# Optimization experiments

Measured on AMD Instinct MI355X. Metric: run time of the kernel, lower is better.

Reference implementation:

```python
import jax, jax.numpy as jnp
import numpy as np

N_NODES = 100000
N_EDGES = 600000
IN_FEATS = 128
HIDDEN = 128


def sage_conv(x, src, dst, w_l, b_l, w_r, num_nodes):
    """PyG SAGEConv with mean aggregation.
    out = mean_{j in N(i)} x_j @ w_l.T + b_l + x_i @ w_r.T
    src/dst: int arrays [E]; messages flow src -> dst.
    """
    msgs = x[src]                                             # [E, F] gather
    summed = jax.ops.segment_sum(msgs, dst, num_segments=num_nodes)  # [N, F]
    ones = jnp.ones((src.shape[0],), dtype=x.dtype)
    deg = jax.ops.segment_sum(ones, dst, num_segments=num_nodes)     # [N]
    agg = summed / jnp.maximum(deg, 1.0)[:, None]             # mean, safe for deg=0
    return agg @ w_l.T + b_l + x @ w_r.T


def setup_inputs() -> dict:
    key = jax.random.key(0)
    ks = jax.random.split(key, 10)

    def glorot(k, shape):
        fan_in = shape[-1]
        bound = 1.0 / np.sqrt(fan_in)
        return jax.random.uniform(k, shape, jnp.float32, -bound, bound)

    x = jax.random.normal(ks[0], (N_NODES, IN_FEATS), dtype=jnp.float32)
    xedge = jax.random.randint(ks[1], (2, N_EDGES), 0, N_NODES, dtype=jnp.int64)
    return {
        "x": x,
        "xedge": xedge,
        # SAGEConv 1 (in_feats -> hidden): lin_l (with bias) + lin_r (no bias)
        "w1_l": glorot(ks[2], (HIDDEN, IN_FEATS)),
        "b1_l": glorot(ks[3], (HIDDEN,)),
        "w1_r": glorot(ks[4], (HIDDEN, IN_FEATS)),
        # SAGEConv 2 (hidden -> hidden)
        "w2_l": glorot(ks[5], (HIDDEN, HIDDEN)),
        "b2_l": glorot(ks[6], (HIDDEN,)),
        "w2_r": glorot(ks[7], (HIDDEN, HIDDEN)),
        # Decoder: Linear(hidden -> hidden)
        "w_dec": glorot(ks[8], (HIDDEN, HIDDEN)),
        "b_dec": glorot(ks[9], (HIDDEN,)),
    }


def reference(x, xedge, w1_l, b1_l, w1_r, w2_l, b2_l, w2_r, w_dec, b_dec):
    src, dst = xedge[0], xedge[1]
    n = x.shape[0]
    h = sage_conv(x, src, dst, w1_l, b1_l, w1_r, n)   # conv1
    h = jax.nn.relu(h)
    # dropout omitted (deterministic eval semantics)
    h = sage_conv(h, src, dst, w2_l, b2_l, w2_r, n)   # conv2 -> encoder output
    dx = h @ w_dec.T + b_dec                          # decoder
    return (h, dx)
```

## Files before the change

### kernel.cpp

```cpp
#include <hip/hip_runtime.h>

typedef __attribute__((ext_vector_type(8))) short bf16x8;
typedef __attribute__((ext_vector_type(4))) float f32x4;
typedef unsigned int uint;
typedef unsigned short ushort;

#define NFEAT 128

__device__ __forceinline__ ushort f2b(float f) {
    uint u = __float_as_uint(f);
    u = (u + 0x7fffu + ((u >> 16) & 1u)) >> 16;
    return (ushort)u;
}

__global__ __launch_bounds__(256) void prep(
    const float* __restrict__ x, ushort* __restrict__ x_bf, long nx,
    const float* __restrict__ w1l, const float* __restrict__ w1r,
    const float* __restrict__ w2l, const float* __restrict__ w2r,
    const float* __restrict__ wd,
    ushort* __restrict__ wc1, ushort* __restrict__ wc2, ushort* __restrict__ wdec,
    const int* __restrict__ dst, int* __restrict__ deg, int E, int nCvt)
{
    const int b = blockIdx.x;
    if (b < nCvt) {
        long i = ((long)b * 256 + threadIdx.x) * 4;
        if (i < nx) {
            float4 v = *(const float4*)(x + i);
            ushort4 o;
            o.x = f2b(v.x); o.y = f2b(v.y); o.z = f2b(v.z); o.w = f2b(v.w);
            *(ushort4*)(x_bf + i) = o;
        }
    } else if (b < nCvt + 256) {
        const int bb = b - nCvt;
        const int i = (bb & 127) * 256 + threadIdx.x;
        const int row = i >> 8, col = i & 255;
        const float* wl = (bb < 128) ? w1l : w2l;
        const float* wr = (bb < 128) ? w1r : w2r;
        ushort* dstw = (bb < 128) ? wc1 : wc2;
        float v = (col < 128) ? wl[row * 128 + col] : wr[row * 128 + col - 128];
        dstw[i] = f2b(v);
    } else if (b < nCvt + 320) {
        const int i = (b - nCvt - 256) * 256 + threadIdx.x;
        wdec[i] = f2b(wd[i]);
    } else {
        const int e = (b - nCvt - 320) * 256 + threadIdx.x;
        if (e < E) atomicAdd(&deg[dst[e]], 1);
    }
}

__global__ __launch_bounds__(256) void scan_blocks(const int* __restrict__ in, int* __restrict__ out,
                                                   int* __restrict__ bsum, int n) {
    __shared__ int lds[256];
    const int t = threadIdx.x;
    const int base = blockIdx.x * 1024 + t * 4;
    int a[4];
#pragma unroll
    for (int q = 0; q < 4; ++q) a[q] = (base + q < n) ? in[base + q] : 0;
    const int tsum = a[0] + a[1] + a[2] + a[3];
    lds[t] = tsum;
    __syncthreads();
    for (int off = 1; off < 256; off <<= 1) {
        int v = (t >= off) ? lds[t - off] : 0;
        __syncthreads();
        lds[t] += v;
        __syncthreads();
    }
    const int excl = lds[t] - tsum;
    if (t == 255) bsum[blockIdx.x] = lds[255];
    int r = excl;
#pragma unroll
    for (int q = 0; q < 4; ++q) {
        if (base + q < n) out[base + q] = r;
        r += a[q];
    }
}

__global__ __launch_bounds__(256) void scan_add(int* __restrict__ row_off, int* __restrict__ pos,
                                                const int* __restrict__ bsum, int n, int E) {
    const int i = blockIdx.x * 256 + threadIdx.x;
    const int cb = blockIdx.x >> 2;
    const int lane = threadIdx.x & 63;
    int v = 0;
    if (lane < cb) v += bsum[lane];
    if (lane + 64 < cb) v += bsum[lane + 64];
#pragma unroll
    for (int off = 1; off < 64; off <<= 1) v += __shfl_xor(v, off);
    if (i < n) {
        const int r = row_off[i] + v;
        row_off[i] = r;
        pos[i] = r;
    }
    if (i == 0) row_off[n] = E;
}

__global__ void fill_csr(const int* __restrict__ src, const int* __restrict__ dst,
                         int* __restrict__ pos, int* __restrict__ perm, int E) {
    const int e = blockIdx.x * blockDim.x + threadIdx.x;
    if (e < E) {
        const int p = atomicAdd(&pos[dst[e]], 1);
        perm[p] = src[e];
    }
}

__global__ __launch_bounds__(256) void gather_mean_bf(const int* __restrict__ row_off,
                                                      const int* __restrict__ perm,
                                                      const ushort* __restrict__ feat,
                                                      ushort* __restrict__ out, int n) {
    const int node = (blockIdx.x * 256 + threadIdx.x) >> 4;
    if (node >= n) return;
    const int chunk = threadIdx.x & 15;
    const int lo = row_off[node], hi = row_off[node + 1];
    float acc[8] = {0.f, 0.f, 0.f, 0.f, 0.f, 0.f, 0.f, 0.f};
    int i = lo;
    for (; i + 3 < hi; i += 4) {
        const int s0 = perm[i], s1 = perm[i + 1], s2 = perm[i + 2], s3 = perm[i + 3];
        const uint4 v0 = *(const uint4*)(feat + (size_t)s0 * NFEAT + chunk * 8);
        const uint4 v1 = *(const uint4*)(feat + (size_t)s1 * NFEAT + chunk * 8);
        const uint4 v2 = *(const uint4*)(feat + (size_t)s2 * NFEAT + chunk * 8);
        const uint4 v3 = *(const uint4*)(feat + (size_t)s3 * NFEAT + chunk * 8);
        const uint p0[4] = {v0.x, v0.y, v0.z, v0.w};
        const uint p1[4] = {v1.x, v1.y, v1.z, v1.w};
        const uint p2[4] = {v2.x, v2.y, v2.z, v2.w};
        const uint p3[4] = {v3.x, v3.y, v3.z, v3.w};
#pragma unroll
        for (int q = 0; q < 4; ++q) {
            acc[2 * q]     += __uint_as_float(p0[q] << 16) + __uint_as_float(p1[q] << 16)
                            + __uint_as_float(p2[q] << 16) + __uint_as_float(p3[q] << 16);
            acc[2 * q + 1] += __uint_as_float(p0[q] & 0xffff0000u) + __uint_as_float(p1[q] & 0xffff0000u)
                            + __uint_as_float(p2[q] & 0xffff0000u) + __uint_as_float(p3[q] & 0xffff0000u);
        }
    }
    for (; i < hi; ++i) {
        const int s = perm[i];
        const uint4 v = *(const uint4*)(feat + (size_t)s * NFEAT + chunk * 8);
        const uint p[4] = {v.x, v.y, v.z, v.w};
#pragma unroll
        for (int q = 0; q < 4; ++q) {
            acc[2 * q]     += __uint_as_float(p[q] << 16);
            acc[2 * q + 1] += __uint_as_float(p[q] & 0xffff0000u);
        }
    }
    const float inv = 1.0f / fmaxf((float)(hi - lo), 1.0f);
    ushort o[8] __attribute__((aligned(16)));
#pragma unroll
    for (int q = 0; q < 8; ++q) o[q] = f2b(acc[q] * inv);
    *(uint4*)(out + (size_t)node * NFEAT + chunk * 8) = *(const uint4*)o;
}

template <bool RELU, bool DEC>
__global__ __launch_bounds__(256) void sage_mfma(
    const ushort* __restrict__ Amean, const ushort* __restrict__ Axin,
    const ushort* __restrict__ Wcat, const float* __restrict__ bias,
    const ushort* __restrict__ Wdec, const float* __restrict__ bdec,
    float* __restrict__ outf, ushort* __restrict__ outb,
    float* __restrict__ dxp, int n)
{
    __shared__ uint4 LhBuf[DEC ? 2048 : 1];
    char* Lh = (char*)LhBuf;
    const int t = threadIdx.x;
    const int m0 = blockIdx.x * 128;
    const int lane = t & 63;
    const int wid = t >> 6;
    const int lrow = lane & 15;
    const int lq = lane >> 4;

    int ar[2];
#pragma unroll
    for (int m = 0; m < 2; ++m) {
        int r = m0 + wid * 32 + m * 16 + lrow;
        ar[m] = (r < n) ? r : (n - 1);
    }

    f32x4 acc[2][8];
#pragma unroll
    for (int m = 0; m < 2; ++m)
#pragma unroll
        for (int nn = 0; nn < 8; ++nn) acc[m][nn] = (f32x4){0.f, 0.f, 0.f, 0.f};

#pragma unroll
    for (int kt = 0; kt < 4; ++kt) {
        const ushort* Abase = (kt < 2) ? Amean : Axin;
        const int co = (kt & 1) * 64;
#pragma unroll
        for (int ks = 0; ks < 2; ++ks) {
            const int kcol = co + ks * 32 + lq * 8;
            bf16x8 af[2], bfr[8];
#pragma unroll
            for (int m = 0; m < 2; ++m)
                af[m] = *(const bf16x8*)(Abase + (size_t)ar[m] * NFEAT + kcol);
#pragma unroll
            for (int nn = 0; nn < 8; ++nn)
                bfr[nn] = *(const bf16x8*)(Wcat + (size_t)(nn * 16 + lrow) * 256 + kt * 64 + ks * 32 + lq * 8);
#pragma unroll
            for (int m = 0; m < 2; ++m)
#pragma unroll
                for (int nn = 0; nn < 8; ++nn)
                    acc[m][nn] = __builtin_amdgcn_mfma_f32_16x16x32_bf16(bfr[nn], af[m], acc[m][nn], 0, 0, 0);
        }
    }

#pragma unroll
    for (int m = 0; m < 2; ++m) {
        const int row = wid * 32 + m * 16 + lrow;
        const int grow = m0 + row;
#pragma unroll
        for (int nn = 0; nn < 8; ++nn) {
            const int colb = nn * 16 + lq * 4;
            const float4 bv = *(const float4*)(bias + colb);
            float v0 = acc[m][nn][0] + bv.x;
            float v1 = acc[m][nn][1] + bv.y;
            float v2 = acc[m][nn][2] + bv.z;
            float v3 = acc[m][nn][3] + bv.w;
            if (RELU) {
                v0 = fmaxf(v0, 0.f); v1 = fmaxf(v1, 0.f);
                v2 = fmaxf(v2, 0.f); v3 = fmaxf(v3, 0.f);
            }
            ushort4 ob;
            ob.x = f2b(v0); ob.y = f2b(v1); ob.z = f2b(v2); ob.w = f2b(v3);
            if (grow < n) {
                if (outf) *(float4*)(outf + (size_t)grow * NFEAT + colb) = make_float4(v0, v1, v2, v3);
                if (outb) *(ushort4*)(outb + (size_t)grow * NFEAT + colb) = ob;
            }
            if (DEC)
                *(ushort4*)(Lh + row * 256 + ((colb * 2) ^ ((row & 7) << 4))) = ob;
        }
    }
    if (DEC) {
        f32x4 acc2[2][8];
#pragma unroll
        for (int m = 0; m < 2; ++m)
#pragma unroll
            for (int nn = 0; nn < 8; ++nn) acc2[m][nn] = (f32x4){0.f, 0.f, 0.f, 0.f};
#pragma unroll
        for (int ks = 0; ks < 4; ++ks) {
            bf16x8 af2[2], bf2[8];
#pragma unroll
            for (int m = 0; m < 2; ++m) {
                const int row = wid * 32 + m * 16 + lrow;
                af2[m] = *(const bf16x8*)(Lh + row * 256 + ((ks * 64 + lq * 16) ^ ((row & 7) << 4)));
            }
#pragma unroll
            for (int nn = 0; nn < 8; ++nn)
                bf2[nn] = *(const bf16x8*)(Wdec + (size_t)(nn * 16 + lrow) * NFEAT + ks * 32 + lq * 8);
#pragma unroll
            for (int m = 0; m < 2; ++m)
#pragma unroll
                for (int nn = 0; nn < 8; ++nn)
                    acc2[m][nn] = __builtin_amdgcn_mfma_f32_16x16x32_bf16(bf2[nn], af2[m], acc2[m][nn], 0, 0, 0);
        }
#pragma unroll
        for (int m = 0; m < 2; ++m) {
            const int grow = m0 + wid * 32 + m * 16 + lrow;
            if (grow < n) {
#pragma unroll
                for (int nn = 0; nn < 8; ++nn) {
                    const int colb = nn * 16 + lq * 4;
                    const float4 bv = *(const float4*)(bdec + colb);
                    *(float4*)(dxp + (size_t)grow * NFEAT + colb) =
                        make_float4(acc2[m][nn][0] + bv.x, acc2[m][nn][1] + bv.y,
                                    acc2[m][nn][2] + bv.z, acc2[m][nn][3] + bv.w);
                }
            }
        }
    }
}

extern "C" void kernel_launch(void* const* d_in, const int* in_sizes, int n_in,
                              void* d_out, int out_size, void* d_ws, size_t ws_size,
                              hipStream_t stream) {
    const float* x     = (const float*)d_in[0];
    const int*   xedge = (const int*)d_in[1];
    const float* w1_l  = (const float*)d_in[2];
    const float* b1_l  = (const float*)d_in[3];
    const float* w1_r  = (const float*)d_in[4];
    const float* w2_l  = (const float*)d_in[5];
    const float* b2_l  = (const float*)d_in[6];
    const float* w2_r  = (const float*)d_in[7];
    const float* w_dec = (const float*)d_in[8];
    const float* b_dec = (const float*)d_in[9];

    const int N = in_sizes[0] / NFEAT;
    const int E = in_sizes[1] / 2;
    const int* src = xedge;
    const int* dst = xedge + E;

    float* h_out = (float*)d_out;
    float* dxp   = h_out + (size_t)N * NFEAT;

    char* ws = (char*)d_ws;
    ushort* x_bf    = (ushort*)ws;
    ushort* h1_bf   = x_bf   + (size_t)N * NFEAT;
    ushort* mean_bf = h1_bf  + (size_t)N * NFEAT;
    ushort* wc1     = mean_bf + (size_t)N * NFEAT;
    ushort* wc2     = wc1 + 128 * 256;
    ushort* wdec    = wc2 + 128 * 256;
    int* deg        = (int*)(wdec + 128 * 128);
    int* row_off    = deg + N;
    int* pos        = row_off + (N + 1);
    int* bsum       = pos + N;
    int* perm       = bsum + 256;

    hipMemsetAsync(deg, 0, (size_t)N * sizeof(int), stream);
    const long nx = (long)N * NFEAT;
    const int nCvt = (int)((nx / 4 + 255) / 256);
    const int histB = (E + 255) / 256;
    prep<<<nCvt + 320 + histB, 256, 0, stream>>>(x, x_bf, nx, w1_l, w1_r, w2_l, w2_r, w_dec,
                                                 wc1, wc2, wdec, dst, deg, E, nCvt);

    const int nb = (N + 1023) / 1024;
    scan_blocks<<<nb, 256, 0, stream>>>(deg, row_off, bsum, N);
    scan_add<<<(N + 255) / 256, 256, 0, stream>>>(row_off, pos, bsum, N, E);
    fill_csr<<<histB, 256, 0, stream>>>(src, dst, pos, perm, E);

    const int gb = (N + 127) / 128;
    const int ggb = (N * 16 + 255) / 256;

    gather_mean_bf<<<ggb, 256, 0, stream>>>(row_off, perm, x_bf, mean_bf, N);
    sage_mfma<true, false><<<gb, 256, 0, stream>>>(mean_bf, x_bf, wc1, b1_l,
                                                   nullptr, nullptr, nullptr, h1_bf, nullptr, N);

    gather_mean_bf<<<ggb, 256, 0, stream>>>(row_off, perm, h1_bf, mean_bf, N);
    sage_mfma<false, true><<<gb, 256, 0, stream>>>(mean_bf, h1_bf, wc2, b2_l,
                                                   wdec, b_dec, h_out, nullptr, dxp, N);

    (void)n_in; (void)out_size; (void)ws_size;
}
```

Baseline: 245.0 us.

## Stage A and weight tiles into swizzled LDS via direct global-to-LDS loads

The MFMA GEMM kernel used to load A-row fragments and weight fragments straight from global memory into registers for each k-step. It now stages a 128x64 A tile and a 128x64 weight tile per k-tile into LDS with global_load_lds, using an XOR swizzle to avoid bank conflicts, then reads the MFMA fragments from LDS. The aim is coalesced, shared weight loads instead of each wave re-fetching the weights. In exchange it adds two barriers per k-tile with no double buffering, and it always allocates 32KB of LDS, which may lower occupancy.

Result: faster. 199.8 us (median of 3 runs) (-18.5%).

```diff
diff --git a/kernel.cpp b/kernel.cpp
--- a/kernel.cpp
+++ b/kernel.cpp
@@ -11,6 +11,11 @@
     uint u = __float_as_uint(f);
     u = (u + 0x7fffu + ((u >> 16) & 1u)) >> 16;
     return (ushort)u;
+}
+
+__device__ __forceinline__ void gload_lds16(const ushort* g, char* lds) {
+    __builtin_amdgcn_global_load_lds((const __attribute__((address_space(1))) void*)g,
+                                     (__attribute__((address_space(3))) void*)lds, 16, 0, 0);
 }
 
 __global__ __launch_bounds__(256) void prep(
@@ -155,8 +160,9 @@
     float* __restrict__ outf, ushort* __restrict__ outb,
     float* __restrict__ dxp, int n)
 {
-    __shared__ uint4 LhBuf[DEC ? 2048 : 1];
-    char* Lh = (char*)LhBuf;
+    __shared__ uint4 smem4[2048];
+    char* As = (char*)smem4;
+    char* Ws = As + 16384;
     const int t = threadIdx.x;
     const int m0 = blockIdx.x * 128;
     const int lane = t & 63;
@@ -164,41 +170,49 @@
     const int lrow = lane & 15;
     const int lq = lane >> 4;
 
-    int ar[2];
-#pragma unroll
-    for (int m = 0; m < 2; ++m) {
-        int r = m0 + wid * 32 + m * 16 + lrow;
-        ar[m] = (r < n) ? r : (n - 1);
-    }
-
     f32x4 acc[2][8];
 #pragma unroll
     for (int m = 0; m < 2; ++m)
 #pragma unroll
         for (int nn = 0; nn < 8; ++nn) acc[m][nn] = (f32x4){0.f, 0.f, 0.f, 0.f};
 
-#pragma unroll
     for (int kt = 0; kt < 4; ++kt) {
         const ushort* Abase = (kt < 2) ? Amean : Axin;
         const int co = (kt & 1) * 64;
 #pragma unroll
+        for (int i = 0; i < 4; ++i) {
+            const int row = i * 32 + wid * 8 + (lane >> 3);
+            const int c = (lane & 7) ^ (row & 7);
+            int gm = m0 + row;
+            if (gm >= n) gm = n - 1;
+            gload_lds16(Abase + (size_t)gm * NFEAT + co + c * 8,
+                        As + i * 4096 + wid * 1024);
+            gload_lds16(Wcat + (size_t)row * 256 + kt * 64 + c * 8,
+                        Ws + i * 4096 + wid * 1024);
+        }
+        __syncthreads();
+#pragma unroll
         for (int ks = 0; ks < 2; ++ks) {
-            const int kcol = co + ks * 32 + lq * 8;
             bf16x8 af[2], bfr[8];
 #pragma unroll
-            for (int m = 0; m < 2; ++m)
-                af[m] = *(const bf16x8*)(Abase + (size_t)ar[m] * NFEAT + kcol);
-#pragma unroll
-            for (int nn = 0; nn < 8; ++nn)
-                bfr[nn] = *(const bf16x8*)(Wcat + (size_t)(nn * 16 + lrow) * 256 + kt * 64 + ks * 32 + lq * 8);
+            for (int m = 0; m < 2; ++m) {
+                const int row = wid * 32 + m * 16 + lrow;
+                af[m] = *(const bf16x8*)(As + row * 128 + (((ks * 4 + lq) * 16) ^ ((row & 7) << 4)));
+            }
+#pragma unroll
+            for (int nn = 0; nn < 8; ++nn) {
+                const int row = nn * 16 + lrow;
+                bfr[nn] = *(const bf16x8*)(Ws + row * 128 + (((ks * 4 + lq) * 16) ^ ((row & 7) << 4)));
+            }
 #pragma unroll
             for (int m = 0; m < 2; ++m)
 #pragma unroll
                 for (int nn = 0; nn < 8; ++nn)
                     acc[m][nn] = __builtin_amdgcn_mfma_f32_16x16x32_bf16(bfr[nn], af[m], acc[m][nn], 0, 0, 0);
         }
-    }
-
+        __syncthreads();
+    }
+    char* Lh = As;
 #pragma unroll
     for (int m = 0; m < 2; ++m) {
         const int row = wid * 32 + m * 16 + lrow;
```
